# Kernel tuning notes

Hardware: AMD Instinct MI355X
Metric: run time of the kernel (lower is better)

The kernel has to match this reference:

```python
import jax, jax.numpy as jnp
import numpy as np

B, C, I = 4096, 256, 16          # nodes, channels (num_features), per-channel irrep dim (lmax=3)
K3, K2, K1 = 23, 4, 1            # num symmetric-contraction paths per correlation order


def setup_inputs() -> dict:
    key = jax.random.key(0)
    ks = jax.random.split(key, 8)
    return {
        "node_feats": jax.random.normal(ks[0], (B, C, I), jnp.float32),
        "U3": jax.random.normal(ks[1], (I, I, I, K3), jnp.float32),  # fixed CG basis, corr=3
        "U2": jax.random.normal(ks[2], (I, I, K2), jnp.float32),     # fixed CG basis, corr=2
        "U1": jax.random.normal(ks[3], (I, K1), jnp.float32),        # fixed CG basis, corr=1
        "w3": jax.random.normal(ks[4], (C, K3), jnp.float32),        # per-channel weights, corr=3
        "w2": jax.random.normal(ks[5], (C, K2), jnp.float32),
        "w1": jax.random.normal(ks[6], (C, K1), jnp.float32),
        "W_lin": jax.random.normal(ks[7], (C, C), jnp.float32),      # o3.Linear (scalars) weight
    }


def reference(node_feats, U3, U2, U1, w3, w2, w1, W_lin):
    """MACE symmetric contraction (ProductBasisBlock), vectorized over channels.

    Per-channel math (correlation = 3):
      out = einsum('pqik,k,bi->bpq', U3, w3[c], x[:,c])          # main
      c2  = einsum('pqk,k->pq', U2, w2[c]); out = einsum('bpi,bi->bp', c2+out, x[:,c])
      c1  = einsum('pk,k->p',  U1, w1[c]); out = einsum('bi,bi->b',  c1+out, x[:,c])
    The Python-level per-channel loop is replaced by a channel axis c in the einsums.
    """
    x = node_feats                                            # (B, C, I)
    # --- main contraction at correlation order 3 ---
    U3w = jnp.einsum('pqik,ck->cpqi', U3, w3)                 # (C, I, I, I)
    out = jnp.einsum('cpqi,bci->bcpq', U3w, x)                # (B, C, I, I)
    # --- corr = 2 ---
    c2 = jnp.einsum('pik,ck->cpi', U2, w2)                    # (C, I, I)
    out = jnp.einsum('bcpi,bci->bcp', c2[None] + out, x)      # (B, C, I)
    # --- corr = 1 ---
    c1 = jnp.einsum('ik,ck->ci', U1, w1)                      # (C, I)
    out = jnp.einsum('bci,bci->bc', c1[None] + out, x)        # (B, C)
    # --- o3.Linear on the scalar (0e) outputs: x @ W with 1/sqrt(fan_in) path norm ---
    inv_sqrt_fan_in = 1.0 / np.sqrt(C).astype(np.float32)
    return jnp.einsum('bc,cd->bd', out, W_lin) * inv_sqrt_fan_in
```

## Files before the change

### kernel.cpp

```cpp
#include <hip/hip_runtime.h>


#define B_NODES 4096
#define C_CH    256
#define K3      23
#define K2      4

#define KSTEPS   9
#define KB_ELEMS (KSTEPS * 64 * 8)
#define KB_U32   (KB_ELEMS / 2)

#define TILES_PER_WAVE 8

typedef short    short8 __attribute__((ext_vector_type(8)));
typedef float    f32x4  __attribute__((ext_vector_type(4)));
typedef unsigned u32x4  __attribute__((ext_vector_type(4)));

static constexpr size_t OFF_BF_BYTES = 0;
static constexpr size_t OFF_ST_BYTES = (size_t)C_CH * KB_ELEMS * 2;

__device__ inline unsigned short f2bf_rne(float f) {
  unsigned u = __builtin_bit_cast(unsigned, f);
  unsigned r = u + 0x7FFFu + ((u >> 16) & 1u);
  return (unsigned short)(r >> 16);
}

#define F2U(f) __builtin_bit_cast(unsigned, (f))
#define PK2(YH, YL) __builtin_amdgcn_perm(F2U(YH), F2U(YL), 0x07060302u)

__global__ __launch_bounds__(256) void precompute_bfrag(
    const float* __restrict__ U3, const float* __restrict__ U2,
    const float* __restrict__ U1, const float* __restrict__ w3,
    const float* __restrict__ w2, const float* __restrict__ w1,
    unsigned int* __restrict__ bfrag_u32) {
  const int s  = blockIdx.x;
  const int c0 = blockIdx.y * 8;
  const int t  = threadIdx.x;
  const int lane = t >> 2;
  const int jj   = (t & 3) * 2;
  const int p = lane & 15, g = lane >> 4;

  __shared__ float su3[512 * 23];

  if (s < 8) {
    for (int l = t; l < 512 * 23; l += 256) {
      const int row = l / 23, col = l - row * 23;
      const int pp = row >> 5, qb = (row >> 4) & 1, ii = row & 15;
      su3[l] = U3[(size_t)((pp * 16 + (2 * s + qb)) * 16 + ii) * K3 + col];
    }
    __syncthreads();

    const int r0 = p * 32 + (g >> 1) * 16 + (g & 1) * 8 + jj;
    float u0[K3], u1[K3];
#pragma unroll
    for (int k3 = 0; k3 < K3; ++k3) {
      u0[k3] = su3[(size_t)r0 * K3 + k3];
      u1[k3] = su3[(size_t)(r0 + 1) * K3 + k3];
    }
#pragma unroll
    for (int ch = 0; ch < 8; ++ch) {
      const int c = c0 + ch;
      float a0 = 0.f, a1 = 0.f;
#pragma unroll
      for (int k3 = 0; k3 < K3; ++k3) {
        const float wv = w3[c * K3 + k3];
        a0 += u0[k3] * wv;
        a1 += u1[k3] * wv;
      }
      bfrag_u32[(size_t)c * KB_U32 + s * 256 + t] =
          (unsigned)f2bf_rne(a0) | ((unsigned)f2bf_rne(a1) << 16);
    }
  } else {
#pragma unroll
    for (int ch = 0; ch < 8; ++ch) {
      const int c = c0 + ch;
      float v0 = 0.f, v1 = 0.f;
#pragma unroll
      for (int e = 0; e < 2; ++e) {
        const int k = 256 + g * 8 + jj + e;
        float a = 0.f;
        if (k < 272) {
          const int q = k - 256;
#pragma unroll
          for (int k2 = 0; k2 < K2; ++k2)
            a += U2[(size_t)(p * 16 + q) * K2 + k2] * w2[c * K2 + k2];
        } else if (k == 272) {
          a = U1[p] * w1[c];
        }
        if (e == 0) v0 = a; else v1 = a;
      }
      bfrag_u32[(size_t)c * KB_U32 + s * 256 + t] =
          (unsigned)f2bf_rne(v0) | ((unsigned)f2bf_rne(v1) << 16);
    }
  }
}


#define QSTEP(BF, XQ, ACC)                                                     \
  __builtin_amdgcn_mfma_f32_16x16x32_bf16((BF),                                \
      __builtin_bit_cast(short8, (u32x4){                                      \
          PK2((XQ) * xh1, (XQ) * xh0), PK2((XQ) * xh3, (XQ) * xh2),            \
          PK2((XQ) * xh5, (XQ) * xh4), PK2((XQ) * xh7, (XQ) * xh6)}),          \
      (ACC), 0, 0, 0)

#define TILE_BODY(X0, X1, X2, X3, Tc)                                          \
  do {                                                                         \
    const float xh0 = ghi ? (X2).x : (X0).x;                                   \
    const float xh1 = ghi ? (X2).y : (X0).y;                                   \
    const float xh2 = ghi ? (X2).z : (X0).z;                                   \
    const float xh3 = ghi ? (X2).w : (X0).w;                                   \
    const float xh4 = ghi ? (X3).x : (X1).x;                                   \
    const float xh5 = ghi ? (X3).y : (X1).y;                                   \
    const float xh6 = ghi ? (X3).z : (X1).z;                                   \
    const float xh7 = ghi ? (X3).w : (X1).w;                                   \
    const float xq0 = gq ? (X0).y : (X0).x;                                    \
    const float xq1 = gq ? (X0).w : (X0).z;                                    \
    const float xq2 = gq ? (X1).y : (X1).x;                                    \
    const float xq3 = gq ? (X1).w : (X1).z;                                    \
    const float xq4 = gq ? (X2).y : (X2).x;                                    \
    const float xq5 = gq ? (X2).w : (X2).z;                                    \
    const float xq6 = gq ? (X3).y : (X3).x;                                    \
    const float xq7 = gq ? (X3).w : (X3).z;                                    \
    f32x4 acc = (f32x4){0.f, 0.f, 0.f, 0.f};                                   \
    acc = QSTEP(bf0, xq0, acc);                                                \
    acc = QSTEP(bf1, xq1, acc);                                                \
    acc = QSTEP(bf2, xq2, acc);                                                \
    acc = QSTEP(bf3, xq3, acc);                                                \
    acc = QSTEP(bf4, xq4, acc);                                                \
    acc = QSTEP(bf5, xq5, acc);                                                \
    acc = QSTEP(bf6, xq6, acc);                                                \
    acc = QSTEP(bf7, xq7, acc);                                                \
    {                                                                          \
      const float y0 = glin ? xh0 : cst;                                       \
      const float y1 = glin ? xh1 : 0.f;                                       \
      const float y2 = glin ? xh2 : 0.f;                                       \
      const float y3 = glin ? xh3 : 0.f;                                       \
      const float y4 = glin ? xh4 : 0.f;                                       \
      const float y5 = glin ? xh5 : 0.f;                                       \
      const float y6 = glin ? xh6 : 0.f;                                       \
      const float y7 = glin ? xh7 : 0.f;                                       \
      acc = __builtin_amdgcn_mfma_f32_16x16x32_bf16(bf8,                       \
          __builtin_bit_cast(short8, (u32x4){PK2(y1, y0), PK2(y3, y2),         \
                                             PK2(y5, y4), PK2(y7, y6)}),       \
          acc, 0, 0, 0);                                                       \
    }                                                                          \
    const float4 xs = (g & 2) ? ((g & 1) ? (X3) : (X2))                        \
                              : ((g & 1) ? (X1) : (X0));                       \
    float v = acc[0] * xs.x + acc[1] * xs.y + acc[2] * xs.z + acc[3] * xs.w;   \
    v += __shfl_xor(v, 16);                                                    \
    v += __shfl_xor(v, 32);                                                    \
    if (g == 0) sTrow[(Tc) * 16 + n] = v;                                      \
  } while (0)

__global__ __launch_bounds__(256)
__attribute__((amdgpu_waves_per_eu(2, 4)))
void contract_mfma(
    const float* __restrict__ x, const short8* __restrict__ bfragv,
    float* __restrict__ sT) {
  const int c0  = blockIdx.x * 4;
  const int nb0 = blockIdx.y * (TILES_PER_WAVE * 16);
  const int t   = threadIdx.x;
  const int w = t >> 6, lane = t & 63, n = lane & 15, g = lane >> 4;
  const int ch = c0 + w;

  const short8* bp = bfragv + (size_t)ch * (KSTEPS * 64);
  const short8 bf0 = bp[0 * 64 + lane];
  const short8 bf1 = bp[1 * 64 + lane];
  const short8 bf2 = bp[2 * 64 + lane];
  const short8 bf3 = bp[3 * 64 + lane];
  const short8 bf4 = bp[4 * 64 + lane];
  const short8 bf5 = bp[5 * 64 + lane];
  const short8 bf6 = bp[6 * 64 + lane];
  const short8 bf7 = bp[7 * 64 + lane];
  const short8 bf8 = bp[8 * 64 + lane];

  const bool  ghi  = (g & 1) != 0;
  const bool  gq   = ((g >> 1) & 1) != 0;
  const bool  glin = (g < 2);
  const float cst  = (g == 2) ? 1.0f : 0.0f;
  float* sTrow = sT + (size_t)ch * B_NODES + nb0;

  const float* xb = x + (size_t)(nb0 + n) * (C_CH * 16) + (size_t)ch * 16;
  const size_t tstride = (size_t)16 * C_CH * 16;

  float4 a0, a1, a2, a3, b0, b1, b2, b3;
  {
    const float4* p = (const float4*)xb;
    a0 = p[0]; a1 = p[1]; a2 = p[2]; a3 = p[3];
  }

#pragma unroll
  for (int TT = 0; TT < TILES_PER_WAVE / 2; ++TT) {
    {
      const float4* p = (const float4*)(xb + (size_t)(2 * TT + 1) * tstride);
      b0 = p[0]; b1 = p[1]; b2 = p[2]; b3 = p[3];
    }
    TILE_BODY(a0, a1, a2, a3, 2 * TT);
    if (TT + 1 < TILES_PER_WAVE / 2) {
      const float4* p = (const float4*)(xb + (size_t)(2 * TT + 2) * tstride);
      a0 = p[0]; a1 = p[1]; a2 = p[2]; a3 = p[3];
    }
    TILE_BODY(b0, b1, b2, b3, 2 * TT + 1);
  }
}

__global__ __launch_bounds__(256) void linear_kernel(
    const float* __restrict__ sT, const float* __restrict__ W,
    float* __restrict__ out) {
  const int b0 = blockIdx.x * 64;
  const int d0 = blockIdx.y * 64;
  const int t  = threadIdx.x;
  const int tx = t & 15;
  const int ty = t >> 4;

  __shared__ float As[16][64];
  __shared__ float Bs[16][64];
  float acc[4][4] = {};

  for (int k0 = 0; k0 < C_CH; k0 += 16) {
    const int kk  = t >> 6;
    const int col = t & 63;
#pragma unroll
    for (int r = 0; r < 4; ++r) {
      As[kk + r * 4][col] = sT[(size_t)(k0 + kk + r * 4) * B_NODES + b0 + col];
      Bs[kk + r * 4][col] = W[(size_t)(k0 + kk + r * 4) * C_CH + d0 + col];
    }
    __syncthreads();
#pragma unroll
    for (int k = 0; k < 16; ++k) {
      float a[4], bv[4];
#pragma unroll
      for (int i = 0; i < 4; ++i) a[i] = As[k][ty * 4 + i];
#pragma unroll
      for (int j = 0; j < 4; ++j) bv[j] = Bs[k][tx * 4 + j];
#pragma unroll
      for (int i = 0; i < 4; ++i)
#pragma unroll
        for (int j = 0; j < 4; ++j) acc[i][j] += a[i] * bv[j];
    }
    __syncthreads();
  }

#pragma unroll
  for (int i = 0; i < 4; ++i) {
    float4 v = make_float4(acc[i][0] * 0.0625f, acc[i][1] * 0.0625f,
                           acc[i][2] * 0.0625f, acc[i][3] * 0.0625f);
    *(float4*)(out + (size_t)(b0 + ty * 4 + i) * C_CH + d0 + tx * 4) = v;
  }
}

extern "C" void kernel_launch(void* const* d_in, const int* in_sizes, int n_in,
                              void* d_out, int out_size, void* d_ws, size_t ws_size,
                              hipStream_t stream) {
  const float* x  = (const float*)d_in[0];
  const float* U3 = (const float*)d_in[1];
  const float* U2 = (const float*)d_in[2];
  const float* U1 = (const float*)d_in[3];
  const float* w3 = (const float*)d_in[4];
  const float* w2 = (const float*)d_in[5];
  const float* w1 = (const float*)d_in[6];
  const float* Wl = (const float*)d_in[7];

  unsigned int* bfrag = (unsigned int*)((char*)d_ws + OFF_BF_BYTES);
  float*        sT    = (float*)((char*)d_ws + OFF_ST_BYTES);
  float*        out   = (float*)d_out;

  precompute_bfrag<<<dim3(KSTEPS, C_CH / 8), dim3(256), 0, stream>>>(
      U3, U2, U1, w3, w2, w1, bfrag);
  contract_mfma<<<dim3(C_CH / 4, B_NODES / (TILES_PER_WAVE * 16)), dim3(256), 0, stream>>>(
      x, (const short8*)bfrag, sT);
  linear_kernel<<<dim3(B_NODES / 64, C_CH / 64), dim3(256), 0, stream>>>(sT, Wl, out);
}
```

Baseline: 154.4 us.

## Interleave two tiles per MFMA chain with split accumulators and deeper prefetch

```diff
diff --git a/kernel.cpp b/kernel.cpp
--- a/kernel.cpp
+++ b/kernel.cpp
@@ -95,73 +95,115 @@
   }
 }
 
-
-#define QSTEP(BF, XQ, ACC)                                                     \
-  __builtin_amdgcn_mfma_f32_16x16x32_bf16((BF),                                \
-      __builtin_bit_cast(short8, (u32x4){                                      \
-          PK2((XQ) * xh1, (XQ) * xh0), PK2((XQ) * xh3, (XQ) * xh2),            \
-          PK2((XQ) * xh5, (XQ) * xh4), PK2((XQ) * xh7, (XQ) * xh6)}),          \
-      (ACC), 0, 0, 0)
-
-#define TILE_BODY(X0, X1, X2, X3, Tc)                                          \
-  do {                                                                         \
-    const float xh0 = ghi ? (X2).x : (X0).x;                                   \
-    const float xh1 = ghi ? (X2).y : (X0).y;                                   \
-    const float xh2 = ghi ? (X2).z : (X0).z;                                   \
-    const float xh3 = ghi ? (X2).w : (X0).w;                                   \
-    const float xh4 = ghi ? (X3).x : (X1).x;                                   \
-    const float xh5 = ghi ? (X3).y : (X1).y;                                   \
-    const float xh6 = ghi ? (X3).z : (X1).z;                                   \
-    const float xh7 = ghi ? (X3).w : (X1).w;                                   \
-    const float xq0 = gq ? (X0).y : (X0).x;                                    \
-    const float xq1 = gq ? (X0).w : (X0).z;                                    \
-    const float xq2 = gq ? (X1).y : (X1).x;                                    \
-    const float xq3 = gq ? (X1).w : (X1).z;                                    \
-    const float xq4 = gq ? (X2).y : (X2).x;                                    \
-    const float xq5 = gq ? (X2).w : (X2).z;                                    \
-    const float xq6 = gq ? (X3).y : (X3).x;                                    \
-    const float xq7 = gq ? (X3).w : (X3).z;                                    \
-    f32x4 acc = (f32x4){0.f, 0.f, 0.f, 0.f};                                   \
-    acc = QSTEP(bf0, xq0, acc);                                                \
-    acc = QSTEP(bf1, xq1, acc);                                                \
-    acc = QSTEP(bf2, xq2, acc);                                                \
-    acc = QSTEP(bf3, xq3, acc);                                                \
-    acc = QSTEP(bf4, xq4, acc);                                                \
-    acc = QSTEP(bf5, xq5, acc);                                                \
-    acc = QSTEP(bf6, xq6, acc);                                                \
-    acc = QSTEP(bf7, xq7, acc);                                                \
-    {                                                                          \
-      const float y0 = glin ? xh0 : cst;                                       \
-      const float y1 = glin ? xh1 : 0.f;                                       \
-      const float y2 = glin ? xh2 : 0.f;                                       \
-      const float y3 = glin ? xh3 : 0.f;                                       \
-      const float y4 = glin ? xh4 : 0.f;                                       \
-      const float y5 = glin ? xh5 : 0.f;                                       \
-      const float y6 = glin ? xh6 : 0.f;                                       \
-      const float y7 = glin ? xh7 : 0.f;                                       \
-      acc = __builtin_amdgcn_mfma_f32_16x16x32_bf16(bf8,                       \
-          __builtin_bit_cast(short8, (u32x4){PK2(y1, y0), PK2(y3, y2),         \
-                                             PK2(y5, y4), PK2(y7, y6)}),       \
-          acc, 0, 0, 0);                                                       \
-    }                                                                          \
-    const float4 xs = (g & 2) ? ((g & 1) ? (X3) : (X2))                        \
-                              : ((g & 1) ? (X1) : (X0));                       \
-    float v = acc[0] * xs.x + acc[1] * xs.y + acc[2] * xs.z + acc[3] * xs.w;   \
-    v += __shfl_xor(v, 16);                                                    \
-    v += __shfl_xor(v, 32);                                                    \
-    if (g == 0) sTrow[(Tc) * 16 + n] = v;                                      \
-  } while (0)
+__device__ __forceinline__ f32x4 qstep(short8 bfv, float xq,
+                                       float h0, float h1, float h2, float h3,
+                                       float h4, float h5, float h6, float h7,
+                                       f32x4 acc) {
+  u32x4 u;
+  u[0] = PK2(xq * h1, xq * h0);
+  u[1] = PK2(xq * h3, xq * h2);
+  u[2] = PK2(xq * h5, xq * h4);
+  u[3] = PK2(xq * h7, xq * h6);
+  return __builtin_amdgcn_mfma_f32_16x16x32_bf16(
+      bfv, __builtin_bit_cast(short8, u), acc, 0, 0, 0);
+}
+
+__device__ __forceinline__ f32x4 lstep(short8 bfv, bool glin, float cst,
+                                       float h0, float h1, float h2, float h3,
+                                       float h4, float h5, float h6, float h7,
+                                       f32x4 acc) {
+  const float y0 = glin ? h0 : cst;
+  const float y1 = glin ? h1 : 0.f;
+  const float y2 = glin ? h2 : 0.f;
+  const float y3 = glin ? h3 : 0.f;
+  const float y4 = glin ? h4 : 0.f;
+  const float y5 = glin ? h5 : 0.f;
+  const float y6 = glin ? h6 : 0.f;
+  const float y7 = glin ? h7 : 0.f;
+  u32x4 u;
+  u[0] = PK2(y1, y0);
+  u[1] = PK2(y3, y2);
+  u[2] = PK2(y5, y4);
+  u[3] = PK2(y7, y6);
+  return __builtin_amdgcn_mfma_f32_16x16x32_bf16(
+      bfv, __builtin_bit_cast(short8, u), acc, 0, 0, 0);
+}
+
+__device__ __forceinline__ void pair_body(
+    short8 bf0, short8 bf1, short8 bf2, short8 bf3, short8 bf4,
+    short8 bf5, short8 bf6, short8 bf7, short8 bf8,
+    float4 a0, float4 a1, float4 a2, float4 a3,
+    float4 b0, float4 b1, float4 b2, float4 b3,
+    bool ghi, bool gq, bool glin, float cst, int g, int n,
+    float* sTrow, int Ta, int Tb) {
+  const float hA0 = ghi ? a2.x : a0.x, hA1 = ghi ? a2.y : a0.y;
+  const float hA2 = ghi ? a2.z : a0.z, hA3 = ghi ? a2.w : a0.w;
+  const float hA4 = ghi ? a3.x : a1.x, hA5 = ghi ? a3.y : a1.y;
+  const float hA6 = ghi ? a3.z : a1.z, hA7 = ghi ? a3.w : a1.w;
+  const float hB0 = ghi ? b2.x : b0.x, hB1 = ghi ? b2.y : b0.y;
+  const float hB2 = ghi ? b2.z : b0.z, hB3 = ghi ? b2.w : b0.w;
+  const float hB4 = ghi ? b3.x : b1.x, hB5 = ghi ? b3.y : b1.y;
+  const float hB6 = ghi ? b3.z : b1.z, hB7 = ghi ? b3.w : b1.w;
+  const float qA0 = gq ? a0.y : a0.x, qA1 = gq ? a0.w : a0.z;
+  const float qA2 = gq ? a1.y : a1.x, qA3 = gq ? a1.w : a1.z;
+  const float qA4 = gq ? a2.y : a2.x, qA5 = gq ? a2.w : a2.z;
+  const float qA6 = gq ? a3.y : a3.x, qA7 = gq ? a3.w : a3.z;
+  const float qB0 = gq ? b0.y : b0.x, qB1 = gq ? b0.w : b0.z;
+  const float qB2 = gq ? b1.y : b1.x, qB3 = gq ? b1.w : b1.z;
+  const float qB4 = gq ? b2.y : b2.x, qB5 = gq ? b2.w : b2.z;
+  const float qB6 = gq ? b3.y : b3.x, qB7 = gq ? b3.w : b3.z;
+
+  f32x4 aA0 = (f32x4){0.f, 0.f, 0.f, 0.f};
+  f32x4 aA1 = (f32x4){0.f, 0.f, 0.f, 0.f};
+  f32x4 aB0 = (f32x4){0.f, 0.f, 0.f, 0.f};
+  f32x4 aB1 = (f32x4){0.f, 0.f, 0.f, 0.f};
+
+  aA0 = qstep(bf0, qA0, hA0, hA1, hA2, hA3, hA4, hA5, hA6, hA7, aA0);
+  aB0 = qstep(bf0, qB0, hB0, hB1, hB2, hB3, hB4, hB5, hB6, hB7, aB0);
+  aA1 = qstep(bf1, qA1, hA0, hA1, hA2, hA3, hA4, hA5, hA6, hA7, aA1);
+  aB1 = qstep(bf1, qB1, hB0, hB1, hB2, hB3, hB4, hB5, hB6, hB7, aB1);
+  aA0 = qstep(bf2, qA2, hA0, hA1, hA2, hA3, hA4, hA5, hA6, hA7, aA0);
+  aB0 = qstep(bf2, qB2, hB0, hB1, hB2, hB3, hB4, hB5, hB6, hB7, aB0);
+  aA1 = qstep(bf3, qA3, hA0, hA1, hA2, hA3, hA4, hA5, hA6, hA7, aA1);
+  aB1 = qstep(bf3, qB3, hB0, hB1, hB2, hB3, hB4, hB5, hB6, hB7, aB1);
+  aA0 = qstep(bf4, qA4, hA0, hA1, hA2, hA3, hA4, hA5, hA6, hA7, aA0);
+  aB0 = qstep(bf4, qB4, hB0, hB1, hB2, hB3, hB4, hB5, hB6, hB7, aB0);
+  aA1 = qstep(bf5, qA5, hA0, hA1, hA2, hA3, hA4, hA5, hA6, hA7, aA1);
+  aB1 = qstep(bf5, qB5, hB0, hB1, hB2, hB3, hB4, hB5, hB6, hB7, aB1);
+  aA0 = qstep(bf6, qA6, hA0, hA1, hA2, hA3, hA4, hA5, hA6, hA7, aA0);
+  aB0 = qstep(bf6, qB6, hB0, hB1, hB2, hB3, hB4, hB5, hB6, hB7, aB0);
+  aA1 = qstep(bf7, qA7, hA0, hA1, hA2, hA3, hA4, hA5, hA6, hA7, aA1);
+  aB1 = qstep(bf7, qB7, hB0, hB1, hB2, hB3, hB4, hB5, hB6, hB7, aB1);
+  aA0 = lstep(bf8, glin, cst, hA0, hA1, hA2, hA3, hA4, hA5, hA6, hA7, aA0);
+  aB0 = lstep(bf8, glin, cst, hB0, hB1, hB2, hB3, hB4, hB5, hB6, hB7, aB0);
+
+  const f32x4 accA = aA0 + aA1;
+  const f32x4 accB = aB0 + aB1;
+
+  const float4 xsA = (g & 2) ? ((g & 1) ? a3 : a2) : ((g & 1) ? a1 : a0);
+  const float4 xsB = (g & 2) ? ((g & 1) ? b3 : b2) : ((g & 1) ? b1 : b0);
+  float vA = accA[0] * xsA.x + accA[1] * xsA.y + accA[2] * xsA.z + accA[3] * xsA.w;
+  float vB = accB[0] * xsB.x + accB[1] * xsB.y + accB[2] * xsB.z + accB[3] * xsB.w;
+  vA += __shfl_xor(vA, 16);
+  vB += __shfl_xor(vB, 16);
+  vA += __shfl_xor(vA, 32);
+  vB += __shfl_xor(vB, 32);
+  if (g == 0) {
+    sTrow[Ta * 16 + n] = vA;
+    sTrow[Tb * 16 + n] = vB;
+  }
+}
 
 __global__ __launch_bounds__(256)
 __attribute__((amdgpu_waves_per_eu(2, 4)))
 void contract_mfma(
     const float* __restrict__ x, const short8* __restrict__ bfragv,
     float* __restrict__ sT) {
-  const int c0  = blockIdx.x * 4;
+  const int cg0 = blockIdx.x * 4;
   const int nb0 = blockIdx.y * (TILES_PER_WAVE * 16);
   const int t   = threadIdx.x;
   const int w = t >> 6, lane = t & 63, n = lane & 15, g = lane >> 4;
-  const int ch = c0 + w;
+  const int ch = cg0 + w;
 
   const short8* bp = bfragv + (size_t)ch * (KSTEPS * 64);
   const short8 bf0 = bp[0 * 64 + lane];
@@ -183,25 +225,44 @@
   const float* xb = x + (size_t)(nb0 + n) * (C_CH * 16) + (size_t)ch * 16;
   const size_t tstride = (size_t)16 * C_CH * 16;
 
-  float4 a0, a1, a2, a3, b0, b1, b2, b3;
+  float4 ra0, ra1, ra2, ra3, rb0, rb1, rb2, rb3;
+  float4 rc0, rc1, rc2, rc3, rd0, rd1, rd2, rd3;
   {
     const float4* p = (const float4*)xb;
-    a0 = p[0]; a1 = p[1]; a2 = p[2]; a3 = p[3];
-  }
-
-#pragma unroll
-  for (int TT = 0; TT < TILES_PER_WAVE / 2; ++TT) {
-    {
-      const float4* p = (const float4*)(xb + (size_t)(2 * TT + 1) * tstride);
-      b0 = p[0]; b1 = p[1]; b2 = p[2]; b3 = p[3];
-    }
-    TILE_BODY(a0, a1, a2, a3, 2 * TT);
-    if (TT + 1 < TILES_PER_WAVE / 2) {
-      const float4* p = (const float4*)(xb + (size_t)(2 * TT + 2) * tstride);
-      a0 = p[0]; a1 = p[1]; a2 = p[2]; a3 = p[3];
-    }
-    TILE_BODY(b0, b1, b2, b3, 2 * TT + 1);
-  }
+    ra0 = p[0]; ra1 = p[1]; ra2 = p[2]; ra3 = p[3];
+    const float4* q = (const float4*)(xb + tstride);
+    rb0 = q[0]; rb1 = q[1]; rb2 = q[2]; rb3 = q[3];
+  }
+  {
+    const float4* p = (const float4*)(xb + 2 * tstride);
+    rc0 = p[0]; rc1 = p[1]; rc2 = p[2]; rc3 = p[3];
+    const float4* q = (const float4*)(xb + 3 * tstride);
+    rd0 = q[0]; rd1 = q[1]; rd2 = q[2]; rd3 = q[3];
+  }
+  pair_body(bf0, bf1, bf2, bf3, bf4, bf5, bf6, bf7, bf8,
+            ra0, ra1, ra2, ra3, rb0, rb1, rb2, rb3,
+            ghi, gq, glin, cst, g, n, sTrow, 0, 1);
+  {
+    const float4* p = (const float4*)(xb + 4 * tstride);
+    ra0 = p[0]; ra1 = p[1]; ra2 = p[2]; ra3 = p[3];
+    const float4* q = (const float4*)(xb + 5 * tstride);
+    rb0 = q[0]; rb1 = q[1]; rb2 = q[2]; rb3 = q[3];
+  }
+  pair_body(bf0, bf1, bf2, bf3, bf4, bf5, bf6, bf7, bf8,
+            rc0, rc1, rc2, rc3, rd0, rd1, rd2, rd3,
+            ghi, gq, glin, cst, g, n, sTrow, 2, 3);
+  {
+    const float4* p = (const float4*)(xb + 6 * tstride);
+    rc0 = p[0]; rc1 = p[1]; rc2 = p[2]; rc3 = p[3];
+    const float4* q = (const float4*)(xb + 7 * tstride);
+    rd0 = q[0]; rd1 = q[1]; rd2 = q[2]; rd3 = q[3];
+  }
+  pair_body(bf0, bf1, bf2, bf3, bf4, bf5, bf6, bf7, bf8,
+            ra0, ra1, ra2, ra3, rb0, rb1, rb2, rb3,
+            ghi, gq, glin, cst, g, n, sTrow, 4, 5);
+  pair_body(bf0, bf1, bf2, bf3, bf4, bf5, bf6, bf7, bf8,
+            rc0, rc1, rc2, rc3, rd0, rd1, rd2, rd3,
+            ghi, gq, glin, cst, g, n, sTrow, 6, 7);
 }
 
 __global__ __launch_bounds__(256) void linear_kernel(
```

After: 205.1 us. 1.33x slower.
